# Performance work log

Measured on AMD Instinct MI355X. Metric: run time of the kernel, lower is better.

The kernel has to match this reference:

```python
import jax, jax.numpy as jnp
import numpy as np

LOG2PI = float(np.log(2.0 * np.pi))

N, M, K = 16384, 4096, 64


def setup_inputs() -> dict:
    key = jax.random.key(0)
    ks = jax.random.split(key, 6)
    x = jax.random.normal(ks[0], (N, M), dtype=jnp.float32)
    noise = jax.random.normal(ks[1], (N, K), dtype=jnp.float32)
    # small init scale so linear outputs stay numerically tame
    W_enc_mu = jax.random.normal(ks[2], (M, K), dtype=jnp.float32) * 0.02
    b_enc_mu = jnp.zeros((K,), dtype=jnp.float32)
    W_enc_sigma = jax.random.normal(ks[3], (M, 1), dtype=jnp.float32) * 0.002
    b_enc_sigma = jnp.ones((1,), dtype=jnp.float32)
    W_dec_mu = jax.random.normal(ks[4], (K, M), dtype=jnp.float32) * 0.02
    b_dec_mu = jnp.zeros((M,), dtype=jnp.float32)
    W_dec_sigma = jax.random.normal(ks[5], (K, 1), dtype=jnp.float32) * 0.002
    b_dec_sigma = jnp.ones((1,), dtype=jnp.float32)
    return dict(x=x, noise=noise, W_enc_mu=W_enc_mu, b_enc_mu=b_enc_mu,
                W_enc_sigma=W_enc_sigma, b_enc_sigma=b_enc_sigma,
                W_dec_mu=W_dec_mu, b_dec_mu=b_dec_mu,
                W_dec_sigma=W_dec_sigma, b_dec_sigma=b_dec_sigma)


def _iso_mvn_logpdf(x, mu, var, d):
    # log N(x; mu, var * I_d), var: [n] per-sample scalar variance
    sq = jnp.sum((x - mu) ** 2, axis=-1)  # [n]
    return -0.5 * (d * LOG2PI + d * jnp.log(var) + sq / var)


def reference(x, noise, W_enc_mu, b_enc_mu, W_enc_sigma, b_enc_sigma,
              W_dec_mu, b_dec_mu, W_dec_sigma, b_dec_sigma):
    n, m = x.shape
    k = W_enc_mu.shape[1]
    # encoder
    z_mu = x @ W_enc_mu + b_enc_mu              # [n, k]
    s_enc = x @ W_enc_sigma + b_enc_sigma       # [n, 1]
    # reparametrize: z = mu + sigma^2 * noise (as in original)
    z = z_mu + (s_enc ** 2) * noise             # [n, k]
    # decoder
    x_mu = z @ W_dec_mu + b_dec_mu              # [n, m]
    s_dec = z @ W_dec_sigma + b_dec_sigma       # [n, 1]
    # original squares sigma then squares again inside _expand_batch_sigma:
    # diagonal covariance value = sigma^4
    var_z = (s_enc[:, 0] ** 4)                  # [n]
    var_x = (s_dec[:, 0] ** 4)                  # [n]
    log_posterior = _iso_mvn_logpdf(z, z_mu, var_z, k)          # [n]
    log_likelihood = _iso_mvn_logpdf(x, x_mu, var_x, m)         # [n]
    log_prior = -0.5 * (k * LOG2PI + jnp.sum(z ** 2, axis=-1))  # [n]
    lb = jnp.sum(log_posterior - log_likelihood - log_prior)
    return lb.reshape(1)
```

## Files before the change

kernel.cpp:

```cpp
#include <hip/hip_runtime.h>
#include <hip/hip_bf16.h>

#define LOG2PI 1.8378770664093453f


typedef __attribute__((ext_vector_type(8))) short bf16x8;
typedef __attribute__((ext_vector_type(4))) float f32x4;

__device__ __forceinline__ unsigned short f2bf(float f) {
    unsigned int u = __builtin_bit_cast(unsigned int, f);
    u += 0x7FFFu + ((u >> 16) & 1u);
    return (unsigned short)(u >> 16);
}
__device__ __forceinline__ short f2bf_s(float f) {
    return (short)__builtin_bit_cast(unsigned short, __float2bfloat16(f));
}
__device__ __forceinline__ void gll16(const void* g, void* l) {
    __builtin_amdgcn_global_load_lds(
        (const __attribute__((address_space(1))) void*)g,
        (__attribute__((address_space(3))) void*)l, 16, 0, 0);
}

__global__ __launch_bounds__(256) void pack_b_kernel(const float* __restrict__ We,
        const float* __restrict__ Wes, const float* __restrict__ Wd,
        const float* __restrict__ bd, unsigned char* __restrict__ Bp) {
    __shared__ float WeL[2048];
    __shared__ float WdL[2048];
    __shared__ float WesL[32], bdL[32];
    const int kt = blockIdx.x;
    const int t = threadIdx.x;
#pragma unroll
    for (int i = 0; i < 2; ++i) {
        int q = t + 256 * i;
        *reinterpret_cast<f32x4*>(WeL + q * 4) =
            *reinterpret_cast<const f32x4*>(We + (size_t)kt * 2048 + q * 4);
    }
#pragma unroll
    for (int i = 0; i < 2; ++i) {
        int f = t + 256 * i;
        int r = f >> 3, s4 = f & 7;
        *reinterpret_cast<f32x4*>(WdL + r * 32 + s4 * 4) =
            *reinterpret_cast<const f32x4*>(Wd + (size_t)r * 4096 + kt * 32 + s4 * 4);
    }
    if (t < 8) {
        *reinterpret_cast<f32x4*>(WesL + t * 4) =
            *reinterpret_cast<const f32x4*>(Wes + kt * 32 + t * 4);
    } else if (t < 16) {
        int q = t - 8;
        *reinterpret_cast<f32x4*>(bdL + q * 4) =
            *reinterpret_cast<const f32x4*>(bd + kt * 32 + q * 4);
    }
    __syncthreads();
#pragma unroll
    for (int i = 0; i < 3; ++i) {
        int cidx = t + 256 * i;
        if (cidx < 576) {
            int col = cidx >> 2, u = cidx & 3;
            int ku = u ^ ((col + (col >> 2)) & 3);
            unsigned short out[8];
#pragma unroll
            for (int j = 0; j < 8; ++j) {
                int ml = ku * 8 + j;
                float v = 0.f;
                if (col < 64)        v = WeL[ml * 64 + col];
                else if (col < 128)  v = WdL[(col - 64) * 32 + ml];
                else if (col == 128) v = WesL[ml];
                else if (col == 129) v = bdL[ml];
                out[j] = f2bf(v);
            }
            *reinterpret_cast<uint4*>(Bp + ((size_t)kt * 576 + cidx) * 16) =
                *reinterpret_cast<uint4*>(out);
        }
    }
}

__global__ __launch_bounds__(256) void prep_g_kernel(const float* __restrict__ Wd,
        const float* __restrict__ bd, float* __restrict__ G,
        float* __restrict__ hv, float* __restrict__ ev) {
    __shared__ float red[256];
    const int b = blockIdx.x, t = threadIdx.x;
    float p = 0.f;
    if (b < 4096) {
        int a = b >> 6, c = b & 63;
        const f32x4* ra = reinterpret_cast<const f32x4*>(Wd + (size_t)a * 4096);
        const f32x4* rc = reinterpret_cast<const f32x4*>(Wd + (size_t)c * 4096);
        for (int j = t; j < 1024; j += 256) {
            f32x4 u = ra[j], v = rc[j];
            p += u[0] * v[0] + u[1] * v[1] + u[2] * v[2] + u[3] * v[3];
        }
    } else if (b < 4160) {
        int a = b - 4096;
        const f32x4* ra = reinterpret_cast<const f32x4*>(Wd + (size_t)a * 4096);
        const f32x4* rb = reinterpret_cast<const f32x4*>(bd);
        for (int j = t; j < 1024; j += 256) {
            f32x4 u = ra[j], v = rb[j];
            p += u[0] * v[0] + u[1] * v[1] + u[2] * v[2] + u[3] * v[3];
        }
    } else {
        const f32x4* rb = reinterpret_cast<const f32x4*>(bd);
        for (int j = t; j < 1024; j += 256) {
            f32x4 v = rb[j];
            p += v[0] * v[0] + v[1] * v[1] + v[2] * v[2] + v[3] * v[3];
        }
    }
    red[t] = p;
    __syncthreads();
    for (int s = 128; s > 0; s >>= 1) { if (t < s) red[t] += red[t + s]; __syncthreads(); }
    if (t == 0) {
        if (b < 4096) G[b] = red[0];
        else if (b < 4160) hv[b - 4096] = red[0];
        else ev[0] = red[0];
    }
}

__global__ __launch_bounds__(256, 3) void gemm_kernel(const float* __restrict__ x,
        const unsigned char* __restrict__ Bp, float* __restrict__ Pp,
        int steps, int kslice, int ppstride) {
    __shared__ __align__(16) char lds[51200];
    const int tid = threadIdx.x;
    const int lane = tid & 63, w = tid >> 6;
    const int wm = w >> 1, wn = w & 1;
    const int l15 = lane & 15, kg = lane >> 4;
    const int rowbase = blockIdx.x * 128;
    const int ks = blockIdx.y;

    const float* xA[4];
#pragma unroll
    for (int i = 0; i < 4; ++i) {
        int q = i * 256 + tid;
        int row = q >> 3, u8 = q & 7;
        int co = (u8 ^ (row & 7)) << 2;
        xA[i] = x + (size_t)(rowbase + row) * 4096 + (size_t)ks * kslice + co;
    }

    f32x4 acc[4][5];
#pragma unroll
    for (int mi = 0; mi < 4; ++mi)
#pragma unroll
        for (int ni = 0; ni < 5; ++ni) acc[mi][ni] = (f32x4){0.f, 0.f, 0.f, 0.f};
    float sxa[4] = {0.f, 0.f, 0.f, 0.f};

#define STAGE(buf, tt) do { \
        const size_t tb_ = (size_t)(ks * steps + (tt)) * 9216; \
        _Pragma("unroll") \
        for (int i_ = 0; i_ < 4; ++i_) \
            gll16(xA[i_] + (tt) * 32, lds + (buf) * 25600 + i_ * 4096 + tid * 16); \
        _Pragma("unroll") \
        for (int j_ = 0; j_ < 2; ++j_) \
            gll16(Bp + tb_ + (size_t)(j_ * 256 + tid) * 16, \
                  lds + (buf) * 25600 + 16384 + (j_ * 256 + tid) * 16); \
        if (kg == 0) \
            gll16(Bp + tb_ + (size_t)(512 + w * 16 + l15) * 16, \
                  lds + (buf) * 25600 + 16384 + (512 + w * 16 + l15) * 16); \
    } while (0)

#define COMPUTE(buf) do { \
        char* A0 = lds + (buf) * 25600; \
        char* B0 = A0 + 16384; \
        bf16x8 bfr[5]; \
        _Pragma("unroll") \
        for (int ni_ = 0; ni_ < 5; ++ni_) { \
            if (wn == 0 || ni_ < 4) { \
                int col_ = wn * 80 + ni_ * 16 + l15; \
                int q_ = (col_ + (col_ >> 2)) & 3; \
                bfr[ni_] = *reinterpret_cast<const bf16x8*>( \
                    B0 + col_ * 64 + ((kg ^ q_) << 4)); \
            } \
        } \
        _Pragma("unroll") \
        for (int mi_ = 0; mi_ < 4; ++mi_) { \
            int row_ = wm * 64 + mi_ * 16 + l15; \
            int e0_ = (kg << 1) ^ (row_ & 7); \
            f32x4 fa_ = *reinterpret_cast<const f32x4*>(A0 + row_ * 128 + (e0_ << 4)); \
            f32x4 fb_ = *reinterpret_cast<const f32x4*>(A0 + row_ * 128 + ((e0_ ^ 1) << 4)); \
            bf16x8 af_; \
            af_[0] = f2bf_s(fa_[0]); af_[1] = f2bf_s(fa_[1]); \
            af_[2] = f2bf_s(fa_[2]); af_[3] = f2bf_s(fa_[3]); \
            af_[4] = f2bf_s(fb_[0]); af_[5] = f2bf_s(fb_[1]); \
            af_[6] = f2bf_s(fb_[2]); af_[7] = f2bf_s(fb_[3]); \
            if (wn == 0) { \
                sxa[mi_] += fa_[0]*fa_[0] + fa_[1]*fa_[1] + fa_[2]*fa_[2] + fa_[3]*fa_[3] \
                          + fb_[0]*fb_[0] + fb_[1]*fb_[1] + fb_[2]*fb_[2] + fb_[3]*fb_[3]; \
            } \
            _Pragma("unroll") \
            for (int ni_ = 0; ni_ < 5; ++ni_) { \
                if (wn == 0 || ni_ < 4) \
                    acc[mi_][ni_] = __builtin_amdgcn_mfma_f32_16x16x32_bf16( \
                        af_, bfr[ni_], acc[mi_][ni_], 0, 0, 0); \
            } \
        } \
    } while (0)

    STAGE(0, 0);
    asm volatile("s_waitcnt vmcnt(0)" ::: "memory");
    __builtin_amdgcn_s_barrier();
    asm volatile("" ::: "memory");
    int cur = 0;
    for (int t = 0; t < steps - 1; ++t) {
        STAGE(cur ^ 1, t + 1);
        asm volatile("s_waitcnt vmcnt(7)" ::: "memory");
        __builtin_amdgcn_s_barrier();
        asm volatile("" ::: "memory");
        COMPUTE(cur);
        asm volatile("" ::: "memory");
        __builtin_amdgcn_s_barrier();
        cur ^= 1;
    }
    asm volatile("s_waitcnt vmcnt(0)" ::: "memory");
    __builtin_amdgcn_s_barrier();
    asm volatile("" ::: "memory");
    COMPUTE(cur);
#undef STAGE
#undef COMPUTE

#pragma unroll
    for (int mi = 0; mi < 4; ++mi) {
        sxa[mi] += __shfl_xor(sxa[mi], 16);
        sxa[mi] += __shfl_xor(sxa[mi], 32);
    }

    float* C = reinterpret_cast<float*>(lds);
#pragma unroll
    for (int pass = 0; pass < 2; ++pass) {
        __syncthreads();
        if (wm == pass) {
#pragma unroll
            for (int mi = 0; mi < 4; ++mi)
#pragma unroll
                for (int ni = 0; ni < 5; ++ni) {
                    if (wn == 0 || ni < 4) {
                        int col = wn * 80 + ni * 16 + l15;
                        if (col != 130) {
#pragma unroll
                            for (int i2 = 0; i2 < 4; ++i2)
                                C[(mi * 16 + kg * 4 + i2) * 148 + col] = acc[mi][ni][i2];
                        }
                    }
                }
        }
        if (wn == 0 && lane < 16) {
#pragma unroll
            for (int mi = 0; mi < 4; ++mi)
                if (wm == pass) C[(mi * 16 + lane) * 148 + 130] = sxa[mi];
        }
        __syncthreads();
#pragma unroll
        for (int i = 0; i < 9; ++i) {
            int idx = tid + 256 * i;
            int r = idx / 36, c4 = idx % 36;
            f32x4 v = *reinterpret_cast<const f32x4*>(C + r * 148 + c4 * 4);
            *reinterpret_cast<f32x4*>(
                Pp + (size_t)(rowbase + pass * 64 + r) * ppstride + ks * 144 + c4 * 4) = v;
        }
    }
}

__global__ __launch_bounds__(256) void phase2_kernel(const float* __restrict__ Pp,
        const float* __restrict__ noise, const float* __restrict__ bem,
        const float* __restrict__ Wds, const float* __restrict__ bes_p,
        const float* __restrict__ bds_p, const float* __restrict__ G,
        const float* __restrict__ hv, const float* __restrict__ ev,
        float* __restrict__ partial, int ksplit, int ppstride) {
    __shared__ float Gl[4096];
    __shared__ float hl[64], wl[64], beml[64];
    __shared__ float zs[4][64];
    __shared__ float red[4];
    int tid = threadIdx.x;
    for (int i = tid; i < 4096; i += 256) Gl[i] = G[i];
    if (tid < 64) { hl[tid] = hv[tid]; wl[tid] = Wds[tid]; beml[tid] = bem[tid]; }
    __syncthreads();
    float bes = bes_p[0], bds = bds_p[0], e = ev[0];
    int wid = tid >> 6, k = tid & 63;
    const int sw = (k & 15) << 2;
    float wacc = 0.f;
#pragma unroll
    for (int rr = 0; rr < 8; ++rr) {
        int row = blockIdx.x * 32 + wid * 8 + rr;
        const float* base = Pp + (size_t)row * ppstride;
        float zmu = beml[k], ck = 0.f, se = bes, dd = 0.f, sx2 = 0.f;
        for (int s = 0; s < ksplit; ++s) {
            const float* b2 = base + s * 144;
            zmu += b2[k]; ck += b2[64 + k];
            se += b2[128]; dd += b2[129]; sx2 += b2[130];
        }
        float nz = noise[(size_t)row * 64 + k];
        float s2 = se * se;
        float z = fmaf(s2, nz, zmu);
        zs[wid][k] = z;
        float t0 = 0.f, t1 = 0.f, t2 = 0.f, t3 = 0.f;
        const float* gr = &Gl[k * 64];
        const float* zr = &zs[wid][0];
#pragma unroll
        for (int jb = 0; jb < 16; ++jb) {
            int p = (jb * 4) ^ sw;
            f32x4 gv = *reinterpret_cast<const f32x4*>(gr + p);
            f32x4 zv = *reinterpret_cast<const f32x4*>(zr + p);
            t0 = fmaf(gv[0], zv[0], t0); t1 = fmaf(gv[1], zv[1], t1);
            t2 = fmaf(gv[2], zv[2], t2); t3 = fmaf(gv[3], zv[3], t3);
        }
        float t = (t0 + t1) + (t2 + t3);
        float ra = z * z;
        float rb = nz * nz;
        float rc = z * wl[k];
        float rd = z * ck;
        float re = z * fmaf(2.f, hl[k], t);
#pragma unroll
        for (int d = 1; d < 64; d <<= 1) {
            ra += __shfl_xor(ra, d); rb += __shfl_xor(rb, d);
            rc += __shfl_xor(rc, d); rd += __shfl_xor(rd, d);
            re += __shfl_xor(re, d);
        }
        float sdec = rc + bds;
        float xxmu = rd + dd;
        float xmu2 = re + e;
        float sq_lik = sx2 - 2.f * xxmu + xmu2;
        float vz = s2 * s2;
        float sd2 = sdec * sdec;
        float vx = sd2 * sd2;
        wacc += 0.5f * (4096.f * LOG2PI + 4096.f * __logf(vx) + sq_lik / vx
                        + ra - 64.f * __logf(vz) - rb);
    }
    if (k == 0) red[wid] = wacc;
    __syncthreads();
    if (tid == 0) partial[blockIdx.x] = red[0] + red[1] + red[2] + red[3];
}

__global__ __launch_bounds__(256) void final_reduce_kernel(const float* __restrict__ partial,
                                                           float* __restrict__ out) {
    __shared__ float red[4];
    int tid = threadIdx.x;
    float v = 0.f;
    for (int i = tid; i < 512; i += 256) v += partial[i];
#pragma unroll
    for (int d = 1; d < 64; d <<= 1) v += __shfl_xor(v, d);
    if ((tid & 63) == 0) red[tid >> 6] = v;
    __syncthreads();
    if (tid == 0) out[0] = red[0] + red[1] + red[2] + red[3];
}

extern "C" void kernel_launch(void* const* d_in, const int* in_sizes, int n_in,
                              void* d_out, int out_size, void* d_ws, size_t ws_size,
                              hipStream_t stream) {
    const float* x     = (const float*)d_in[0];
    const float* noise = (const float*)d_in[1];
    const float* We    = (const float*)d_in[2];
    const float* bem   = (const float*)d_in[3];
    const float* Wes   = (const float*)d_in[4];
    const float* bes   = (const float*)d_in[5];
    const float* Wd    = (const float*)d_in[6];
    const float* bdm   = (const float*)d_in[7];
    const float* Wds   = (const float*)d_in[8];
    const float* bds   = (const float*)d_in[9];

    int ksplit = (ws_size >= 39340544ull) ? 4 : (ws_size >= 20466176ull ? 2 : 1);
    int steps = 128 / ksplit;
    int kslice = steps * 32;
    int ppstride = ksplit * 144;

    char* ws = (char*)d_ws;
    size_t ppbytes = (size_t)16384 * ppstride * 4;
    float* Pp           = (float*)ws;
    unsigned char* Bp   = (unsigned char*)(ws + ppbytes);
    float* G            = (float*)(ws + ppbytes + 1572864);
    float* hv           = (float*)(ws + ppbytes + 1572864 + 16384);
    float* ev           = (float*)(ws + ppbytes + 1572864 + 16640);
    float* partial      = (float*)(ws + ppbytes + 1572864 + 16896);

    pack_b_kernel<<<128, 256, 0, stream>>>(We, Wes, Wd, bdm, Bp);
    prep_g_kernel<<<4161, 256, 0, stream>>>(Wd, bdm, G, hv, ev);
    gemm_kernel<<<dim3(128, ksplit), 256, 0, stream>>>(x, Bp, Pp, steps, kslice, ppstride);
    phase2_kernel<<<512, 256, 0, stream>>>(Pp, noise, bem, Wds, bes, bds, G, hv, ev,
                                           partial, ksplit, ppstride);
    final_reduce_kernel<<<1, 256, 0, stream>>>(partial, (float*)d_out);
}
```

Measured before the change: 114.2 us.

## Triple-buffer GEMM loads, stagger k-start per block, merge prep kernels

The GEMM main loop moves from double to triple buffering in LDS (76.8KB, launch bound lowered to 2 blocks/CU), keeping two stages of global->LDS loads in flight. Each block also starts its k-loop at a rotated phase, spreading concurrent blocks across different memory regions. The two small prep kernels are merged into one launch to cut launch overhead. The trade-off is lower occupancy from the larger LDS footprint, and the rotated k-order changes the floating-point accumulation order.

```diff
diff --git a/kernel.cpp b/kernel.cpp
--- a/kernel.cpp
+++ b/kernel.cpp
@@ -21,64 +21,63 @@
         (__attribute__((address_space(3))) void*)l, 16, 0, 0);
 }
 
-__global__ __launch_bounds__(256) void pack_b_kernel(const float* __restrict__ We,
+__global__ __launch_bounds__(256) void prep_kernel(const float* __restrict__ We,
         const float* __restrict__ Wes, const float* __restrict__ Wd,
-        const float* __restrict__ bd, unsigned char* __restrict__ Bp) {
+        const float* __restrict__ bd, unsigned char* __restrict__ Bp,
+        float* __restrict__ G, float* __restrict__ hv, float* __restrict__ ev) {
     __shared__ float WeL[2048];
     __shared__ float WdL[2048];
     __shared__ float WesL[32], bdL[32];
-    const int kt = blockIdx.x;
+    __shared__ float red[256];
     const int t = threadIdx.x;
-#pragma unroll
-    for (int i = 0; i < 2; ++i) {
-        int q = t + 256 * i;
-        *reinterpret_cast<f32x4*>(WeL + q * 4) =
-            *reinterpret_cast<const f32x4*>(We + (size_t)kt * 2048 + q * 4);
-    }
-#pragma unroll
-    for (int i = 0; i < 2; ++i) {
-        int f = t + 256 * i;
-        int r = f >> 3, s4 = f & 7;
-        *reinterpret_cast<f32x4*>(WdL + r * 32 + s4 * 4) =
-            *reinterpret_cast<const f32x4*>(Wd + (size_t)r * 4096 + kt * 32 + s4 * 4);
-    }
-    if (t < 8) {
-        *reinterpret_cast<f32x4*>(WesL + t * 4) =
-            *reinterpret_cast<const f32x4*>(Wes + kt * 32 + t * 4);
-    } else if (t < 16) {
-        int q = t - 8;
-        *reinterpret_cast<f32x4*>(bdL + q * 4) =
-            *reinterpret_cast<const f32x4*>(bd + kt * 32 + q * 4);
-    }
-    __syncthreads();
-#pragma unroll
-    for (int i = 0; i < 3; ++i) {
-        int cidx = t + 256 * i;
-        if (cidx < 576) {
-            int col = cidx >> 2, u = cidx & 3;
-            int ku = u ^ ((col + (col >> 2)) & 3);
-            unsigned short out[8];
-#pragma unroll
-            for (int j = 0; j < 8; ++j) {
-                int ml = ku * 8 + j;
-                float v = 0.f;
-                if (col < 64)        v = WeL[ml * 64 + col];
-                else if (col < 128)  v = WdL[(col - 64) * 32 + ml];
-                else if (col == 128) v = WesL[ml];
-                else if (col == 129) v = bdL[ml];
-                out[j] = f2bf(v);
+    if (blockIdx.x < 128) {
+        const int kt = blockIdx.x;
+#pragma unroll
+        for (int i = 0; i < 2; ++i) {
+            int q = t + 256 * i;
+            *reinterpret_cast<f32x4*>(WeL + q * 4) =
+                *reinterpret_cast<const f32x4*>(We + (size_t)kt * 2048 + q * 4);
+        }
+#pragma unroll
+        for (int i = 0; i < 2; ++i) {
+            int f = t + 256 * i;
+            int r = f >> 3, s4 = f & 7;
+            *reinterpret_cast<f32x4*>(WdL + r * 32 + s4 * 4) =
+                *reinterpret_cast<const f32x4*>(Wd + (size_t)r * 4096 + kt * 32 + s4 * 4);
+        }
+        if (t < 8) {
+            *reinterpret_cast<f32x4*>(WesL + t * 4) =
+                *reinterpret_cast<const f32x4*>(Wes + kt * 32 + t * 4);
+        } else if (t < 16) {
+            int q = t - 8;
+            *reinterpret_cast<f32x4*>(bdL + q * 4) =
+                *reinterpret_cast<const f32x4*>(bd + kt * 32 + q * 4);
+        }
+        __syncthreads();
+#pragma unroll
+        for (int i = 0; i < 3; ++i) {
+            int cidx = t + 256 * i;
+            if (cidx < 576) {
+                int col = cidx >> 2, u = cidx & 3;
+                int ku = u ^ ((col + (col >> 2)) & 3);
+                unsigned short out[8];
+#pragma unroll
+                for (int j = 0; j < 8; ++j) {
+                    int ml = ku * 8 + j;
+                    float v = 0.f;
+                    if (col < 64)        v = WeL[ml * 64 + col];
+                    else if (col < 128)  v = WdL[(col - 64) * 32 + ml];
+                    else if (col == 128) v = WesL[ml];
+                    else if (col == 129) v = bdL[ml];
+                    out[j] = f2bf(v);
+                }
+                *reinterpret_cast<uint4*>(Bp + ((size_t)kt * 576 + cidx) * 16) =
+                    *reinterpret_cast<uint4*>(out);
             }
-            *reinterpret_cast<uint4*>(Bp + ((size_t)kt * 576 + cidx) * 16) =
-                *reinterpret_cast<uint4*>(out);
-        }
-    }
-}
-
-__global__ __launch_bounds__(256) void prep_g_kernel(const float* __restrict__ Wd,
-        const float* __restrict__ bd, float* __restrict__ G,
-        float* __restrict__ hv, float* __restrict__ ev) {
-    __shared__ float red[256];
-    const int b = blockIdx.x, t = threadIdx.x;
+        }
+        return;
+    }
+    const int b = blockIdx.x - 128;
     float p = 0.f;
     if (b < 4096) {
         int a = b >> 6, c = b & 63;
@@ -113,10 +112,10 @@
     }
 }
 
-__global__ __launch_bounds__(256, 3) void gemm_kernel(const float* __restrict__ x,
+__global__ __launch_bounds__(256, 2) void gemm_kernel(const float* __restrict__ x,
         const unsigned char* __restrict__ Bp, float* __restrict__ Pp,
         int steps, int kslice, int ppstride) {
-    __shared__ __align__(16) char lds[51200];
+    __shared__ __align__(16) char lds[76800];
     const int tid = threadIdx.x;
     const int lane = tid & 63, w = tid >> 6;
     const int wm = w >> 1, wn = w & 1;
@@ -141,17 +140,18 @@
     float sxa[4] = {0.f, 0.f, 0.f, 0.f};
 
 #define STAGE(buf, tt) do { \
+        char* Lb_ = lds + (buf) * 25600; \
         const size_t tb_ = (size_t)(ks * steps + (tt)) * 9216; \
         _Pragma("unroll") \
         for (int i_ = 0; i_ < 4; ++i_) \
-            gll16(xA[i_] + (tt) * 32, lds + (buf) * 25600 + i_ * 4096 + tid * 16); \
+            gll16(xA[i_] + (tt) * 32, Lb_ + i_ * 4096 + tid * 16); \
         _Pragma("unroll") \
         for (int j_ = 0; j_ < 2; ++j_) \
             gll16(Bp + tb_ + (size_t)(j_ * 256 + tid) * 16, \
-                  lds + (buf) * 25600 + 16384 + (j_ * 256 + tid) * 16); \
+                  Lb_ + 16384 + (j_ * 256 + tid) * 16); \
         if (kg == 0) \
             gll16(Bp + tb_ + (size_t)(512 + w * 16 + l15) * 16, \
-                  lds + (buf) * 25600 + 16384 + (512 + w * 16 + l15) * 16); \
+                  Lb_ + 16384 + (512 + w * 16 + l15) * 16); \
     } while (0)
 
 #define COMPUTE(buf) do { \
@@ -191,25 +191,30 @@
         } \
     } while (0)
 
-    STAGE(0, 0);
-    asm volatile("s_waitcnt vmcnt(0)" ::: "memory");
-    __builtin_amdgcn_s_barrier();
-    asm volatile("" ::: "memory");
+    const int phase = (blockIdx.x + ks * 8) & (steps - 1);
+    int tp0 = phase;
+    int tpn = (tp0 + 1 == steps) ? 0 : tp0 + 1;
+    STAGE(0, tp0);
+    STAGE(1, tpn);
     int cur = 0;
-    for (int t = 0; t < steps - 1; ++t) {
-        STAGE(cur ^ 1, t + 1);
-        asm volatile("s_waitcnt vmcnt(7)" ::: "memory");
+    for (int t = 0; t < steps; ++t) {
+        if (t + 2 < steps) {
+            tpn = (tpn + 1 == steps) ? 0 : tpn + 1;
+            int b2 = (cur == 0) ? 2 : cur - 1;
+            STAGE(b2, tpn);
+            asm volatile("s_waitcnt vmcnt(14)" ::: "memory");
+        } else if (t + 2 == steps) {
+            asm volatile("s_waitcnt vmcnt(7)" ::: "memory");
+        } else {
+            asm volatile("s_waitcnt vmcnt(0)" ::: "memory");
+        }
         __builtin_amdgcn_s_barrier();
         asm volatile("" ::: "memory");
         COMPUTE(cur);
         asm volatile("" ::: "memory");
         __builtin_amdgcn_s_barrier();
-        cur ^= 1;
-    }
-    asm volatile("s_waitcnt vmcnt(0)" ::: "memory");
-    __builtin_amdgcn_s_barrier();
-    asm volatile("" ::: "memory");
-    COMPUTE(cur);
+        cur = (cur == 2) ? 0 : cur + 1;
+    }
 #undef STAGE
 #undef COMPUTE
 
@@ -366,8 +371,7 @@
     float* ev           = (float*)(ws + ppbytes + 1572864 + 16640);
     float* partial      = (float*)(ws + ppbytes + 1572864 + 16896);
 
-    pack_b_kernel<<<128, 256, 0, stream>>>(We, Wes, Wd, bdm, Bp);
-    prep_g_kernel<<<4161, 256, 0, stream>>>(Wd, bdm, G, hv, ev);
+    prep_kernel<<<4289, 256, 0, stream>>>(We, Wes, Wd, bdm, Bp, G, hv, ev);
     gemm_kernel<<<dim3(128, ksplit), 256, 0, stream>>>(x, Bp, Pp, steps, kslice, ppstride);
     phase2_kernel<<<512, 256, 0, stream>>>(Pp, noise, bem, Wds, bes, bds, G, hv, ev,
                                            partial, ksplit, ppstride);
```

After: 101.5 us. 11.1% less time.
